# Performance work log

Hardware: AMD Instinct MI355X
Metric: run time of the kernel (lower is better)

The kernel has to match this reference:

```python
import jax, jax.numpy as jnp
import numpy as np

N = 50000      # nodes
E = 600000     # edges
D = 128        # embedding_dim
H = 256        # GENConv MLP hidden = 2*D (expansion=2, num_layers=2)
L = 2          # n_layers
EPS_MSG = 1e-7
EPS_NORM = 1e-5


def setup_inputs() -> dict:
    key = jax.random.key(0)
    ks = jax.random.split(key, 16)
    s = 0.05
    inp = {}
    inp["x"] = jax.random.normal(ks[0], (N, 1), jnp.float32)
    inp["edge_index"] = jax.random.randint(ks[1], (2, E), 0, N)
    inp["edge_attr"] = jax.random.normal(ks[2], (E, 1), jnp.float32)
    # encoders
    inp["Wn"] = jax.random.normal(ks[3], (1, D), jnp.float32) * s
    inp["bn_b"] = jnp.zeros((D,), jnp.float32)
    inp["We"] = jax.random.normal(ks[4], (1, D), jnp.float32) * s
    inp["be"] = jnp.zeros((D,), jnp.float32)
    # per-layer BatchNorm affine
    inp["bn_gamma"] = jnp.ones((L, D), jnp.float32)
    inp["bn_beta"] = jnp.zeros((L, D), jnp.float32)
    # per-layer GENConv params: learnable temperature t, MLP [D->H->D] with LayerNorm
    inp["t"] = jnp.ones((L,), jnp.float32)
    inp["W1"] = jax.random.normal(ks[5], (L, D, H), jnp.float32) * s
    inp["b1"] = jnp.zeros((L, H), jnp.float32)
    inp["ln_g"] = jnp.ones((L, H), jnp.float32)
    inp["ln_b"] = jnp.zeros((L, H), jnp.float32)
    inp["W2"] = jax.random.normal(ks[6], (L, H, D), jnp.float32) * s
    inp["b2"] = jnp.zeros((L, D), jnp.float32)
    return inp


def _segment_softmax(logits, seg, num):
    # per-channel softmax over edges grouped by destination node
    m = jax.ops.segment_max(logits, seg, num_segments=num)
    m = jnp.where(jnp.isfinite(m), m, 0.0)  # empty segments
    ex = jnp.exp(logits - m[seg])
    den = jax.ops.segment_sum(ex, seg, num_segments=num)
    return ex / (den[seg] + 1e-16)


def reference(x, edge_index, edge_attr, Wn, bn_b, We, be,
              bn_gamma, bn_beta, t, W1, b1, ln_g, ln_b, W2, b2):
    src, dst = edge_index[0], edge_index[1]
    h = x @ Wn + bn_b                 # [N, D] node encoder
    e = edge_attr @ We + be           # [E, D] edge encoder
    for l in range(L):
        # DeepGCNLayer 'res+': h_in -> BN -> ReLU -> conv -> + h_in
        mu = h.mean(axis=0)
        var = h.var(axis=0)
        hn = (h - mu) / jnp.sqrt(var + EPS_NORM) * bn_gamma[l] + bn_beta[l]
        hn = jax.nn.relu(hn)
        # GENConv: msg = relu(x_j + e) + eps; softmax-aggr with temperature t
        msg = jax.nn.relu(hn[src] + e) + EPS_MSG          # [E, D]
        alpha = _segment_softmax(msg * t[l], dst, N)      # [E, D]
        agg = jax.ops.segment_sum(msg * alpha, dst, num_segments=N)  # [N, D]
        out = agg + hn                                    # add root
        # GENConv MLP: Linear -> LayerNorm -> ReLU -> Linear
        z = out @ W1[l] + b1[l]
        zm = z.mean(axis=-1, keepdims=True)
        zv = z.var(axis=-1, keepdims=True)
        z = (z - zm) / jnp.sqrt(zv + EPS_NORM) * ln_g[l] + ln_b[l]
        z = jax.nn.relu(z)
        z = z @ W2[l] + b2[l]
        h = h + z                                         # res+ residual
    # DotProductPredictor over the same edge list
    return (h[src] * h[dst]).sum(axis=-1)                 # [E]
```

## Files before the change

### kernel.cpp

```cpp
#include <hip/hip_runtime.h>
#include <hip/hip_bf16.h>
#include <math.h>

#define NN 50000
#define NE 600000
#define MPAD 50048
#define NHS (MPAD / 16)
#define DIM 128
#define HID 256
#define NB 49
#define HIST_BLOCKS ((NE + 255) / 256)
#define CAST_BLOCKS ((4 * DIM * HID) / 256)
#define EPS_MSG 1e-7f
#define EPS_NORM 1e-5f
#define MLPW_WAVES 3
#define MLPW_THREADS (MLPW_WAVES * 64)

typedef __attribute__((ext_vector_type(8))) short short8v;
typedef __attribute__((ext_vector_type(8))) unsigned short ushort8v;
typedef __attribute__((ext_vector_type(4))) float f32x4;

__device__ inline ushort f2bf(float f) {
    union { float f; unsigned u; } v; v.f = f;
    unsigned r = v.u + 0x7FFF + ((v.u >> 16) & 1);
    return (ushort)(r >> 16);
}
__device__ inline float bf2f(ushort u) {
    union { unsigned u; float f; } v; v.u = (unsigned)u << 16; return v.f;
}

__global__ __launch_bounds__(256) void k_setup(const float* __restrict__ x,
                                               const int* __restrict__ dst,
                                               const float* __restrict__ W1,
                                               const float* __restrict__ W2,
                                               float* __restrict__ xs,
                                               int* __restrict__ deg,
                                               ushort* __restrict__ W1t,
                                               ushort* __restrict__ W2t) {
    int b = blockIdx.x;
    if (b < 64) {
        int lane = threadIdx.x & 63;
        float s = 0.f, q = 0.f;
        for (int i = b * 256 + threadIdx.x; i < NN; i += 64 * 256) {
            float v = x[i];
            s += v; q += v * v;
        }
        #pragma unroll
        for (int off = 32; off >= 1; off >>= 1) {
            s += __shfl_xor(s, off, 64);
            q += __shfl_xor(q, off, 64);
        }
        if (lane == 0) { atomicAdd(&xs[0], s); atomicAdd(&xs[1], q); }
    } else if (b < 64 + HIST_BLOCKS) {
        int i = (b - 64) * 256 + threadIdx.x;
        if (i < NE) atomicAdd(&deg[dst[i]], 1);
    } else {
        const int chunk = DIM * HID;
        int i = (b - 64 - HIST_BLOCKS) * 256 + threadIdx.x;
        int w = i / chunk;
        int j = i - w * chunk;
        if (w < 2) {
            int r = j / HID, c = j - r * HID;
            W1t[(size_t)w * chunk + (size_t)c * DIM + r] = f2bf(W1[(size_t)w * chunk + j]);
        } else {
            int l = w - 2;
            int r = j / DIM, c = j - r * DIM;
            W2t[(size_t)l * chunk + (size_t)c * HID + r] = f2bf(W2[(size_t)l * chunk + j]);
        }
    }
}

__global__ void k_hn0(const float* __restrict__ x, const float* __restrict__ xs,
                      const float* __restrict__ Wn, const float* __restrict__ bnb,
                      const float* __restrict__ gamma, const float* __restrict__ beta,
                      ushort* __restrict__ hn, int total4) {
    int i = blockIdx.x * blockDim.x + threadIdx.x;
    if (i >= total4) return;
    int d4 = (i & 31) * 4;
    int n = i >> 5;
    float mx = xs[0] * (1.f / NN);
    float vx = xs[1] * (1.f / NN) - mx * mx;
    float xv = x[n];
    float4 w = *(const float4*)(Wn + d4);
    float4 b = *(const float4*)(bnb + d4);
    float4 g = *(const float4*)(gamma + d4);
    float4 bt = *(const float4*)(beta + d4);
    ushort4 o;
    {
        float mu = fmaf(mx, w.x, b.x), sc = rsqrtf(vx * w.x * w.x + EPS_NORM) * g.x;
        o.x = f2bf(fmaxf(fmaf(fmaf(xv, w.x, b.x) - mu, sc, bt.x), 0.f));
    }
    {
        float mu = fmaf(mx, w.y, b.y), sc = rsqrtf(vx * w.y * w.y + EPS_NORM) * g.y;
        o.y = f2bf(fmaxf(fmaf(fmaf(xv, w.y, b.y) - mu, sc, bt.y), 0.f));
    }
    {
        float mu = fmaf(mx, w.z, b.z), sc = rsqrtf(vx * w.z * w.z + EPS_NORM) * g.z;
        o.z = f2bf(fmaxf(fmaf(fmaf(xv, w.z, b.z) - mu, sc, bt.z), 0.f));
    }
    {
        float mu = fmaf(mx, w.w, b.w), sc = rsqrtf(vx * w.w * w.w + EPS_NORM) * g.w;
        o.w = f2bf(fmaxf(fmaf(fmaf(xv, w.w, b.w) - mu, sc, bt.w), 0.f));
    }
    *(ushort4*)(hn + (size_t)n * DIM + d4) = o;
}

__global__ __launch_bounds__(256) void k_scanA(const int* __restrict__ deg,
                                               int* __restrict__ partials, int n) {
    __shared__ int ws[4];
    int b = blockIdx.x;
    int t = threadIdx.x;
    int s = 0;
    #pragma unroll
    for (int i = 0; i < 4; ++i) {
        int idx = b * 1024 + t + i * 256;
        s += (idx < n) ? deg[idx] : 0;
    }
    #pragma unroll
    for (int off = 32; off >= 1; off >>= 1) s += __shfl_xor(s, off, 64);
    if ((t & 63) == 0) ws[t >> 6] = s;
    __syncthreads();
    if (t == 0) partials[b] = ws[0] + ws[1] + ws[2] + ws[3];
}

__global__ __launch_bounds__(64) void k_scanB(const int* __restrict__ partials,
                                              int* __restrict__ base,
                                              int* __restrict__ row_off) {
    int t = threadIdx.x;
    int v = (t < NB) ? partials[t] : 0;
    int x = v;
    #pragma unroll
    for (int off = 1; off < 64; off <<= 1) {
        int y = __shfl_up(x, off, 64);
        if (t >= off) x += y;
    }
    if (t < NB) base[t] = x - v;
    if (t == 0) row_off[NN] = NE;
}

__global__ __launch_bounds__(1024) void k_scanC(const int* __restrict__ deg,
                                                const int* __restrict__ base,
                                                int* __restrict__ row_off,
                                                int* __restrict__ cursor, int n) {
    __shared__ int wsum[16];
    int i = blockIdx.x * 1024 + threadIdx.x;
    int lane = threadIdx.x & 63;
    int wid = threadIdx.x >> 6;
    int v = (i < n) ? deg[i] : 0;
    int x = v;
    #pragma unroll
    for (int off = 1; off < 64; off <<= 1) {
        int y = __shfl_up(x, off, 64);
        if (lane >= off) x += y;
    }
    if (lane == 63) wsum[wid] = x;
    __syncthreads();
    if (wid == 0 && lane < 16) {
        int w = wsum[lane];
        #pragma unroll
        for (int off = 1; off < 16; off <<= 1) {
            int y = __shfl_up(w, off, 64);
            if (lane >= off) w += y;
        }
        wsum[lane] = w;
    }
    __syncthreads();
    int prev = (wid == 0) ? 0 : wsum[wid - 1];
    int excl = base[blockIdx.x] + prev + (x - v);
    if (i < n) { row_off[i] = excl; cursor[i] = excl; }
}

__global__ void k_scatter(const int* __restrict__ src, const int* __restrict__ dst,
                          const float* __restrict__ eattr, int* __restrict__ cursor,
                          unsigned long long* __restrict__ erec, int E) {
    int i = blockIdx.x * blockDim.x + threadIdx.x;
    if (i >= E) return;
    int d = dst[i];
    int pos = atomicAdd(&cursor[d], 1);
    unsigned long long r = (unsigned long long)(unsigned)src[i]
                         | ((unsigned long long)(unsigned)i << 16)
                         | ((unsigned long long)f2bf(eattr[i]) << 36);
    erec[pos] = r;
}

__global__ void k_bn_relu(const ushort* __restrict__ hb, const float* __restrict__ stats,
                          const float* __restrict__ gamma, const float* __restrict__ beta,
                          ushort* __restrict__ hn, int total4) {
    int i = blockIdx.x * blockDim.x + threadIdx.x;
    if (i >= total4) return;
    int d4 = (i & 31) * 4;
    int n = i >> 5;
    ushort4 hv = *(const ushort4*)(hb + (size_t)n * DIM + d4);
    float4 s = *(const float4*)(stats + d4);
    float4 q = *(const float4*)(stats + DIM + d4);
    float4 g = *(const float4*)(gamma + d4);
    float4 bt = *(const float4*)(beta + d4);
    ushort4 o;
    {
        float mu = s.x * (1.f / NN), var = q.x * (1.f / NN) - mu * mu;
        float sc = rsqrtf(var + EPS_NORM) * g.x;
        o.x = f2bf(fmaxf(fmaf(bf2f(hv.x) - mu, sc, bt.x), 0.f));
    }
    {
        float mu = s.y * (1.f / NN), var = q.y * (1.f / NN) - mu * mu;
        float sc = rsqrtf(var + EPS_NORM) * g.y;
        o.y = f2bf(fmaxf(fmaf(bf2f(hv.y) - mu, sc, bt.y), 0.f));
    }
    {
        float mu = s.z * (1.f / NN), var = q.z * (1.f / NN) - mu * mu;
        float sc = rsqrtf(var + EPS_NORM) * g.z;
        o.z = f2bf(fmaxf(fmaf(bf2f(hv.z) - mu, sc, bt.z), 0.f));
    }
    {
        float mu = s.w * (1.f / NN), var = q.w * (1.f / NN) - mu * mu;
        float sc = rsqrtf(var + EPS_NORM) * g.w;
        o.w = f2bf(fmaxf(fmaf(bf2f(hv.w) - mu, sc, bt.w), 0.f));
    }
    *(ushort4*)(hn + (size_t)n * DIM + d4) = o;
}

__global__ __launch_bounds__(256) void k_agg(const ushort* __restrict__ hn,
                                             const unsigned long long* __restrict__ erec,
                                             const int* __restrict__ row_off,
                                             const float* __restrict__ We,
                                             const float* __restrict__ be,
                                             const float* __restrict__ t_all, int l,
                                             ushort* __restrict__ ob, int N) {
    int n = blockIdx.x * 4 + (threadIdx.x >> 6);
    if (n >= N) return;
    int lane = threadIdx.x & 63;
    int d0 = lane * 2;
    float2 we = *(const float2*)(We + d0);
    float2 bd = *(const float2*)(be + d0);
    float t = t_all[l];
    int p0 = row_off[n], p1 = row_off[n + 1];
    int deg = p1 - p0;

    int mp = p0 + lane;
    unsigned long long r_l = (mp < p1) ? erec[mp] : 0ull;

    float den0 = 0.f, num0 = 0.f, den1 = 0.f, num1 = 0.f;
    int kmax = deg < 64 ? deg : 64;
    int k = 0;
    for (; k + 8 <= kmax; k += 8) {
        int ss[8]; float ee[8]; uint hv[8];
        #pragma unroll
        for (int u = 0; u < 8; ++u) {
            unsigned long long r = __shfl(r_l, k + u, 64);
            ss[u] = (int)(r & 0xFFFF);
            ee[u] = bf2f((ushort)(r >> 36));
        }
        #pragma unroll
        for (int u = 0; u < 8; ++u)
            hv[u] = *(const uint*)(hn + (size_t)ss[u] * DIM + d0);
        #pragma unroll
        for (int u = 0; u < 8; ++u) {
            float m0 = fmaxf(bf2f((ushort)hv[u]) + fmaf(ee[u], we.x, bd.x), 0.f) + EPS_MSG;
            float m1 = fmaxf(bf2f((ushort)(hv[u] >> 16)) + fmaf(ee[u], we.y, bd.y), 0.f) + EPS_MSG;
            float x0 = __expf(m0 * t), x1 = __expf(m1 * t);
            den0 += x0; num0 += m0 * x0; den1 += x1; num1 += m1 * x1;
        }
    }
    for (; k < kmax; ++k) {
        unsigned long long r = __shfl(r_l, k, 64);
        int s = (int)(r & 0xFFFF);
        float ea = bf2f((ushort)(r >> 36));
        uint hv = *(const uint*)(hn + (size_t)s * DIM + d0);
        float m0 = fmaxf(bf2f((ushort)hv) + fmaf(ea, we.x, bd.x), 0.f) + EPS_MSG;
        float m1 = fmaxf(bf2f((ushort)(hv >> 16)) + fmaf(ea, we.y, bd.y), 0.f) + EPS_MSG;
        float x0 = __expf(m0 * t), x1 = __expf(m1 * t);
        den0 += x0; num0 += m0 * x0; den1 += x1; num1 += m1 * x1;
    }
    for (int p = p0 + 64; p < p1; ++p) {
        unsigned long long r = erec[p];
        int s = (int)(r & 0xFFFF);
        float ea = bf2f((ushort)(r >> 36));
        uint hv = *(const uint*)(hn + (size_t)s * DIM + d0);
        float m0 = fmaxf(bf2f((ushort)hv) + fmaf(ea, we.x, bd.x), 0.f) + EPS_MSG;
        float m1 = fmaxf(bf2f((ushort)(hv >> 16)) + fmaf(ea, we.y, bd.y), 0.f) + EPS_MSG;
        float x0 = __expf(m0 * t), x1 = __expf(m1 * t);
        den0 += x0; num0 += m0 * x0; den1 += x1; num1 += m1 * x1;
    }
    uint hr = *(const uint*)(hn + (size_t)n * DIM + d0);
    float a0 = (deg > 0) ? num0 / (den0 + 1e-16f) : 0.f;
    float a1 = (deg > 0) ? num1 / (den1 + 1e-16f) : 0.f;
    uint o = (uint)f2bf(a0 + bf2f((ushort)hr)) |
             ((uint)f2bf(a1 + bf2f((ushort)(hr >> 16))) << 16);
    *(uint*)(ob + (size_t)n * DIM + d0) = o;
}

template <int FIRST>
__global__ __launch_bounds__(MLPW_THREADS, 1) void k_mlpw(const ushort* __restrict__ A,
                                                          const ushort* __restrict__ B1t,
                                                          const float* __restrict__ b1,
                                                          const float* __restrict__ g,
                                                          const float* __restrict__ bv,
                                                          const ushort* __restrict__ B2t,
                                                          const float* __restrict__ b2,
                                                          const float* __restrict__ x,
                                                          const float* __restrict__ Wn,
                                                          const float* __restrict__ bnb,
                                                          const ushort* hbin,
                                                          ushort* hbout,
                                                          float* __restrict__ stats) {
    __shared__ ushort W1s[256 * 128];
    __shared__ ushort W2s[128 * 256];
    __shared__ ushort Zs[MLPW_WAVES][16 * 256];
    const int tid = threadIdx.x;
    const int lane = tid & 63;
    const int wid = tid >> 6;
    const int l15 = lane & 15;
    const int lq = lane >> 4;
    char* const w1b = (char*)W1s;
    char* const w2b = (char*)W2s;
    char* const zb = (char*)Zs[wid];

    for (int c = tid; c < 4096; c += MLPW_THREADS) {
        int r = c >> 4;
        int cb = (c & 15) * 16;
        *(short8v*)(w1b + r * 256 + (cb ^ ((r & 15) << 4))) =
            *(const short8v*)(B1t + r * 128 + cb / 2);
    }
    for (int c = tid; c < 4096; c += MLPW_THREADS) {
        int r = c >> 5;
        int cb = (c & 31) * 16;
        *(short8v*)(w2b + r * 512 + (cb ^ ((r & 15) << 4))) =
            *(const short8v*)(B2t + r * 256 + cb / 2);
    }
    float bb[16], gg[16], lb[16];
    #pragma unroll
    for (int nf = 0; nf < 16; ++nf) {
        int col = nf * 16 + l15;
        bb[nf] = b1[col]; gg[nf] = g[col]; lb[nf] = bv[col];
    }
    float b2v[8], wnc[8], bnc[8];
    #pragma unroll
    for (int nf = 0; nf < 8; ++nf) {
        int col = nf * 16 + l15;
        b2v[nf] = b2[col];
        wnc[nf] = FIRST ? Wn[col] : 0.f;
        bnc[nf] = FIRST ? bnb[col] : 0.f;
    }
    float ss[8] = {}, sqv[8] = {};
    __syncthreads();

    for (int hs = blockIdx.x * MLPW_WAVES + wid; hs < NHS; hs += 256 * MLPW_WAVES) {
        const int row0 = hs * 16;
        short8v afr[4];
        #pragma unroll
        for (int ks = 0; ks < 4; ++ks)
            afr[ks] = *(const short8v*)(A + (size_t)(row0 + l15) * DIM + ks * 32 + lq * 8);
        f32x4 acc[16] = {};
        #pragma unroll
        for (int ks = 0; ks < 4; ++ks) {
            int cb = (ks * 64 + lq * 16) ^ (l15 << 4);
            #pragma unroll
            for (int nf = 0; nf < 16; ++nf) {
                short8v bfr = *(const short8v*)(w1b + (nf * 16 + l15) * 256 + cb);
                acc[nf] = __builtin_amdgcn_mfma_f32_16x16x32_bf16(afr[ks], bfr, acc[nf],
                                                                  0, 0, 0);
            }
        }
        #pragma unroll
        for (int j = 0; j < 4; ++j) {
            float sum = 0.f, sq = 0.f;
            #pragma unroll
            for (int nf = 0; nf < 16; ++nf) {
                float v = acc[nf][j] + bb[nf];
                acc[nf][j] = v;
                sum += v; sq += v * v;
            }
            #pragma unroll
            for (int off = 1; off <= 8; off <<= 1) {
                sum += __shfl_xor(sum, off, 64);
                sq += __shfl_xor(sq, off, 64);
            }
            float mu = sum * (1.f / HID);
            float var = sq * (1.f / HID) - mu * mu;
            float rs = rsqrtf(var + EPS_NORM);
            int row = lq * 4 + j;
            #pragma unroll
            for (int nf = 0; nf < 16; ++nf) {
                float v = fmaxf(fmaf((acc[nf][j] - mu) * rs, gg[nf], lb[nf]), 0.f);
                int cbz = ((nf * 16 + l15) * 2) ^ ((row & 15) << 4);
                *(ushort*)(zb + row * 512 + cbz) = f2bf(v);
            }
        }
        short8v az[8];
        #pragma unroll
        for (int ks = 0; ks < 8; ++ks)
            az[ks] = *(const short8v*)(zb + l15 * 512 + ((ks * 64 + lq * 16) ^ (l15 << 4)));
        f32x4 acc2[8] = {};
        #pragma unroll
        for (int ks = 0; ks < 8; ++ks) {
            int cb = (ks * 64 + lq * 16) ^ (l15 << 4);
            #pragma unroll
            for (int nf = 0; nf < 8; ++nf) {
                short8v bfr = *(const short8v*)(w2b + (nf * 16 + l15) * 512 + cb);
                acc2[nf] = __builtin_amdgcn_mfma_f32_16x16x32_bf16(az[ks], bfr, acc2[nf],
                                                                   0, 0, 0);
            }
        }
        #pragma unroll
        for (int j = 0; j < 4; ++j) {
            int gr = row0 + lq * 4 + j;
            float xb = 0.f;
            if (FIRST) xb = (gr < NN) ? x[gr] : 0.f;
            size_t rbase = (size_t)gr * DIM;
            bool ok = gr < NN;
            #pragma unroll
            for (int nf = 0; nf < 8; ++nf) {
                int col = nf * 16 + l15;
                float base = FIRST ? fmaf(xb, wnc[nf], bnc[nf]) : bf2f(hbin[rbase + col]);
                float v = acc2[nf][j] + b2v[nf] + base;
                hbout[rbase + col] = f2bf(v);
                if (FIRST) {
                    ss[nf] += ok ? v : 0.f;
                    sqv[nf] += ok ? v * v : 0.f;
                }
            }
        }
    }
    if (FIRST) {
        #pragma unroll
        for (int nf = 0; nf < 8; ++nf) {
            float s = ss[nf], q = sqv[nf];
            s += __shfl_xor(s, 16, 64); s += __shfl_xor(s, 32, 64);
            q += __shfl_xor(q, 16, 64); q += __shfl_xor(q, 32, 64);
            if (lq == 0) {
                int col = nf * 16 + l15;
                atomicAdd(&stats[col], s);
                atomicAdd(&stats[DIM + col], q);
            }
        }
    }
}

__global__ __launch_bounds__(256) void k_dot(const ushort* __restrict__ hb,
                                             const unsigned long long* __restrict__ erec,
                                             const int* __restrict__ row_off,
                                             float* __restrict__ out, int N) {
    int n = blockIdx.x * 4 + (threadIdx.x >> 6);
    if (n >= N) return;
    int lane = threadIdx.x & 63;
    int sub = lane >> 4;
    int l16 = lane & 15;
    float hd[8];
    {
        ushort8v hv = *(const ushort8v*)(hb + (size_t)n * DIM + l16 * 8);
        #pragma unroll
        for (int j = 0; j < 8; ++j) hd[j] = bf2f(hv[j]);
    }
    int p0 = row_off[n], p1 = row_off[n + 1];
    int deg = p1 - p0;
    int mp = p0 + lane;
    unsigned long long r_l = (mp < p1) ? erec[mp] : 0ull;
    int kmax = deg < 64 ? deg : 64;
    for (int k = 0; k < kmax; k += 4) {
        int idx = k + sub;
        bool ok = idx < kmax;
        unsigned long long r = __shfl(r_l, idx, 64);
        int s = (int)(r & 0xFFFF);
        int e = (int)((r >> 16) & 0xFFFFF);
        ushort8v av = *(const ushort8v*)(hb + (size_t)(ok ? s : n) * DIM + l16 * 8);
        float p = 0.f;
        #pragma unroll
        for (int j = 0; j < 8; ++j) p = fmaf(bf2f(av[j]), hd[j], p);
        p += __shfl_xor(p, 1, 16);
        p += __shfl_xor(p, 2, 16);
        p += __shfl_xor(p, 4, 16);
        p += __shfl_xor(p, 8, 16);
        if (ok && l16 == 0) out[e] = p;
    }
    for (int pb = p0 + 64; pb < p1; pb += 4) {
        int pe = pb + sub;
        bool ok = pe < p1;
        int s = n, e = 0;
        if (ok) {
            unsigned long long r = erec[pe];
            s = (int)(r & 0xFFFF);
            e = (int)((r >> 16) & 0xFFFFF);
        }
        ushort8v av = *(const ushort8v*)(hb + (size_t)s * DIM + l16 * 8);
        float p = 0.f;
        #pragma unroll
        for (int j = 0; j < 8; ++j) p = fmaf(bf2f(av[j]), hd[j], p);
        p += __shfl_xor(p, 1, 16);
        p += __shfl_xor(p, 2, 16);
        p += __shfl_xor(p, 4, 16);
        p += __shfl_xor(p, 8, 16);
        if (ok && l16 == 0) out[e] = p;
    }
}

extern "C" void kernel_launch(void* const* d_in, const int* in_sizes, int n_in,
                              void* d_out, int out_size, void* d_ws, size_t ws_size,
                              hipStream_t stream) {
    const float* x        = (const float*)d_in[0];
    const int*   ei       = (const int*)d_in[1];
    const float* eattr    = (const float*)d_in[2];
    const float* Wn       = (const float*)d_in[3];
    const float* bnb      = (const float*)d_in[4];
    const float* We       = (const float*)d_in[5];
    const float* be       = (const float*)d_in[6];
    const float* bn_gamma = (const float*)d_in[7];
    const float* bn_beta  = (const float*)d_in[8];
    const float* t_all    = (const float*)d_in[9];
    const float* W1       = (const float*)d_in[10];
    const float* b1       = (const float*)d_in[11];
    const float* ln_g     = (const float*)d_in[12];
    const float* ln_b     = (const float*)d_in[13];
    const float* W2       = (const float*)d_in[14];
    const float* b2       = (const float*)d_in[15];
    float* out = (float*)d_out;

    const int N = NN, E = NE, D = DIM, H = HID;
    const int* src = ei;
    const int* dst = ei + E;

    char* ws = (char*)d_ws;
    auto alloc = [&](size_t bytes) {
        char* p = ws;
        ws += (bytes + 255) & ~(size_t)255;
        return p;
    };
    ushort* ob      = (ushort*)alloc((size_t)MPAD * D * 2);
    ushort* hn      = (ushort*)alloc((size_t)MPAD * D * 2);
    ushort* hb      = (ushort*)alloc((size_t)MPAD * D * 2);
    ushort* W1t     = (ushort*)alloc((size_t)2 * D * H * 2);
    ushort* W2t     = (ushort*)alloc((size_t)2 * D * H * 2);
    unsigned long long* erec = (unsigned long long*)alloc((size_t)E * 8);
    int*    row_off = (int*)alloc((size_t)(N + 1) * 4);
    int*    cursor  = (int*)alloc((size_t)N * 4);
    int*    deg     = (int*)alloc((size_t)N * 4);
    int*    partials= (int*)alloc((size_t)64 * 4);
    int*    pbase   = (int*)alloc((size_t)64 * 4);
    float*  stats   = (float*)alloc((size_t)2 * D * 4);
    float*  xs      = (float*)alloc((size_t)2 * 4);

    hipMemsetAsync(deg, 0, (size_t)N * 4, stream);
    hipMemsetAsync(stats, 0, 1024 + 8, stream);

    k_setup<<<64 + HIST_BLOCKS + CAST_BLOCKS, 256, 0, stream>>>(x, dst, W1, W2,
                                                                xs, deg, W1t, W2t);
    k_scanA<<<NB, 256, 0, stream>>>(deg, partials, N);
    k_scanB<<<1, 64, 0, stream>>>(partials, pbase, row_off);
    k_scanC<<<NB, 1024, 0, stream>>>(deg, pbase, row_off, cursor, N);
    k_scatter<<<(E + 255) / 256, 256, 0, stream>>>(src, dst, eattr, cursor, erec, E);
    k_hn0<<<(N * 32 + 255) / 256, 256, 0, stream>>>(x, xs, Wn, bnb, bn_gamma, bn_beta,
                                                    hn, N * 32);

    k_agg<<<(N + 3) / 4, 256, 0, stream>>>(hn, erec, row_off, We, be, t_all, 0, ob, N);
    k_mlpw<1><<<256, MLPW_THREADS, 0, stream>>>(ob, W1t, b1, ln_g, ln_b, W2t, b2,
                                                x, Wn, bnb, hb, hb, stats);
    k_bn_relu<<<(N * 32 + 255) / 256, 256, 0, stream>>>(hb, stats, bn_gamma + D,
                                                        bn_beta + D, hn, N * 32);

    k_agg<<<(N + 3) / 4, 256, 0, stream>>>(hn, erec, row_off, We, be, t_all, 1, ob, N);
    k_mlpw<0><<<256, MLPW_THREADS, 0, stream>>>(ob, W1t + (size_t)D * H, b1 + H,
                                                ln_g + H, ln_b + H, W2t + (size_t)D * H,
                                                b2 + D, x, Wn, bnb, hb, hb, stats);

    k_dot<<<(N + 3) / 4, 256, 0, stream>>>(hb, erec, row_off, out, N);
}
```

Baseline: 431.4 us.

## Split fused MLP kernel into two GEMM kernels with global intermediate

```diff
diff --git a/kernel.cpp b/kernel.cpp
--- a/kernel.cpp
+++ b/kernel.cpp
@@ -13,8 +13,6 @@
 #define CAST_BLOCKS ((4 * DIM * HID) / 256)
 #define EPS_MSG 1e-7f
 #define EPS_NORM 1e-5f
-#define MLPW_WAVES 3
-#define MLPW_THREADS (MLPW_WAVES * 64)
 
 typedef __attribute__((ext_vector_type(8))) short short8v;
 typedef __attribute__((ext_vector_type(8))) unsigned short ushort8v;
@@ -289,147 +287,169 @@
     *(uint*)(ob + (size_t)n * DIM + d0) = o;
 }
 
-template <int FIRST>
-__global__ __launch_bounds__(MLPW_THREADS, 1) void k_mlpw(const ushort* __restrict__ A,
-                                                          const ushort* __restrict__ B1t,
-                                                          const float* __restrict__ b1,
-                                                          const float* __restrict__ g,
-                                                          const float* __restrict__ bv,
-                                                          const ushort* __restrict__ B2t,
-                                                          const float* __restrict__ b2,
-                                                          const float* __restrict__ x,
-                                                          const float* __restrict__ Wn,
-                                                          const float* __restrict__ bnb,
-                                                          const ushort* hbin,
-                                                          ushort* hbout,
-                                                          float* __restrict__ stats) {
+__global__ __launch_bounds__(512, 4) void k_z1(const ushort* __restrict__ A,
+                                               const ushort* __restrict__ B1t,
+                                               const float* __restrict__ b1,
+                                               ushort* __restrict__ z,
+                                               float2* __restrict__ murs) {
     __shared__ ushort W1s[256 * 128];
-    __shared__ ushort W2s[128 * 256];
-    __shared__ ushort Zs[MLPW_WAVES][16 * 256];
     const int tid = threadIdx.x;
     const int lane = tid & 63;
     const int wid = tid >> 6;
     const int l15 = lane & 15;
     const int lq = lane >> 4;
     char* const w1b = (char*)W1s;
-    char* const w2b = (char*)W2s;
-    char* const zb = (char*)Zs[wid];
-
-    for (int c = tid; c < 4096; c += MLPW_THREADS) {
+
+    for (int c = tid; c < 4096; c += 512) {
         int r = c >> 4;
         int cb = (c & 15) * 16;
         *(short8v*)(w1b + r * 256 + (cb ^ ((r & 15) << 4))) =
             *(const short8v*)(B1t + r * 128 + cb / 2);
     }
-    for (int c = tid; c < 4096; c += MLPW_THREADS) {
+    __syncthreads();
+
+    int s = blockIdx.x * 8 + wid;
+    if (s >= NHS) return;
+    const int row0 = s * 16;
+
+    short8v afr[4];
+    #pragma unroll
+    for (int ks = 0; ks < 4; ++ks)
+        afr[ks] = *(const short8v*)(A + (size_t)(row0 + l15) * DIM + ks * 32 + lq * 8);
+
+    float rsum[4] = {}, rsq[4] = {};
+    ushort* zrow = z + (size_t)(row0 + lq * 4) * HID + l15;
+    #pragma unroll
+    for (int ct = 0; ct < 16; ++ct) {
+        f32x4 acc = {};
+        int cb = 0 ^ (l15 << 4);
+        #pragma unroll
+        for (int ks = 0; ks < 4; ++ks) {
+            short8v bfr = *(const short8v*)(w1b + (ct * 16 + l15) * 256 +
+                                            ((ks * 64 + lq * 16) ^ (l15 << 4)));
+            acc = __builtin_amdgcn_mfma_f32_16x16x32_bf16(afr[ks], bfr, acc, 0, 0, 0);
+        }
+        (void)cb;
+        float bbv = b1[ct * 16 + l15];
+        #pragma unroll
+        for (int j = 0; j < 4; ++j) {
+            float zv = acc[j] + bbv;
+            rsum[j] += zv; rsq[j] += zv * zv;
+            zrow[(size_t)j * HID + ct * 16] = f2bf(zv);
+        }
+    }
+    #pragma unroll
+    for (int j = 0; j < 4; ++j) {
+        float sm = rsum[j], q = rsq[j];
+        sm += __shfl_xor(sm, 1, 16); q += __shfl_xor(q, 1, 16);
+        sm += __shfl_xor(sm, 2, 16); q += __shfl_xor(q, 2, 16);
+        sm += __shfl_xor(sm, 4, 16); q += __shfl_xor(q, 4, 16);
+        sm += __shfl_xor(sm, 8, 16); q += __shfl_xor(q, 8, 16);
+        if (l15 == 0) {
+            float mu = sm * (1.f / HID);
+            float var = q * (1.f / HID) - mu * mu;
+            murs[row0 + lq * 4 + j] = make_float2(mu, rsqrtf(var + EPS_NORM));
+        }
+    }
+}
+
+template <int FIRST>
+__global__ __launch_bounds__(512, 4) void k_z2(const ushort* __restrict__ z,
+                                               const float2* __restrict__ murs,
+                                               const float* __restrict__ g,
+                                               const float* __restrict__ lb,
+                                               const ushort* __restrict__ B2t,
+                                               const float* __restrict__ b2,
+                                               const float* __restrict__ x,
+                                               const float* __restrict__ Wn,
+                                               const float* __restrict__ bnb,
+                                               const ushort* hbin,
+                                               ushort* hbout,
+                                               float* __restrict__ stats) {
+    __shared__ ushort W2s[128 * 256];
+    const int tid = threadIdx.x;
+    const int lane = tid & 63;
+    const int wid = tid >> 6;
+    const int l15 = lane & 15;
+    const int lq = lane >> 4;
+    char* const w2b = (char*)W2s;
+
+    for (int c = tid; c < 4096; c += 512) {
         int r = c >> 5;
         int cb = (c & 31) * 16;
         *(short8v*)(w2b + r * 512 + (cb ^ ((r & 15) << 4))) =
             *(const short8v*)(B2t + r * 256 + cb / 2);
     }
-    float bb[16], gg[16], lb[16];
-    #pragma unroll
-    for (int nf = 0; nf < 16; ++nf) {
-        int col = nf * 16 + l15;
-        bb[nf] = b1[col]; gg[nf] = g[col]; lb[nf] = bv[col];
-    }
-    float b2v[8], wnc[8], bnc[8];
-    #pragma unroll
-    for (int nf = 0; nf < 8; ++nf) {
-        int col = nf * 16 + l15;
-        b2v[nf] = b2[col];
-        wnc[nf] = FIRST ? Wn[col] : 0.f;
-        bnc[nf] = FIRST ? bnb[col] : 0.f;
-    }
+    __syncthreads();
+
+    int s = blockIdx.x * 8 + wid;
+    if (s >= NHS) return;
+    const int row0 = s * 16;
+
+    float2 mr = murs[row0 + l15];
+    short8v af2[8];
+    #pragma unroll
+    for (int ks = 0; ks < 8; ++ks) {
+        ushort8v zr = *(const ushort8v*)(z + (size_t)(row0 + l15) * HID + ks * 32 + lq * 8);
+        float4 g0 = *(const float4*)(g + ks * 32 + lq * 8);
+        float4 g1 = *(const float4*)(g + ks * 32 + lq * 8 + 4);
+        float4 l0 = *(const float4*)(lb + ks * 32 + lq * 8);
+        float4 l1 = *(const float4*)(lb + ks * 32 + lq * 8 + 4);
+        ushort8v o;
+        o[0] = f2bf(fmaxf(fmaf((bf2f(zr[0]) - mr.x) * mr.y, g0.x, l0.x), 0.f));
+        o[1] = f2bf(fmaxf(fmaf((bf2f(zr[1]) - mr.x) * mr.y, g0.y, l0.y), 0.f));
+        o[2] = f2bf(fmaxf(fmaf((bf2f(zr[2]) - mr.x) * mr.y, g0.z, l0.z), 0.f));
+        o[3] = f2bf(fmaxf(fmaf((bf2f(zr[3]) - mr.x) * mr.y, g0.w, l0.w), 0.f));
+        o[4] = f2bf(fmaxf(fmaf((bf2f(zr[4]) - mr.x) * mr.y, g1.x, l1.x), 0.f));
+        o[5] = f2bf(fmaxf(fmaf((bf2f(zr[5]) - mr.x) * mr.y, g1.y, l1.y), 0.f));
+        o[6] = f2bf(fmaxf(fmaf((bf2f(zr[6]) - mr.x) * mr.y, g1.z, l1.z), 0.f));
+        o[7] = f2bf(fmaxf(fmaf((bf2f(zr[7]) - mr.x) * mr.y, g1.w, l1.w), 0.f));
+        af2[ks] = (short8v)o;
+    }
+
     float ss[8] = {}, sqv[8] = {};
-    __syncthreads();
-
-    for (int hs = blockIdx.x * MLPW_WAVES + wid; hs < NHS; hs += 256 * MLPW_WAVES) {
-        const int row0 = hs * 16;
-        short8v afr[4];
-        #pragma unroll
-        for (int ks = 0; ks < 4; ++ks)
-            afr[ks] = *(const short8v*)(A + (size_t)(row0 + l15) * DIM + ks * 32 + lq * 8);
-        f32x4 acc[16] = {};
-        #pragma unroll
-        for (int ks = 0; ks < 4; ++ks) {
-            int cb = (ks * 64 + lq * 16) ^ (l15 << 4);
-            #pragma unroll
-            for (int nf = 0; nf < 16; ++nf) {
-                short8v bfr = *(const short8v*)(w1b + (nf * 16 + l15) * 256 + cb);
-                acc[nf] = __builtin_amdgcn_mfma_f32_16x16x32_bf16(afr[ks], bfr, acc[nf],
-                                                                  0, 0, 0);
-            }
-        }
-        #pragma unroll
-        for (int j = 0; j < 4; ++j) {
-            float sum = 0.f, sq = 0.f;
-            #pragma unroll
-            for (int nf = 0; nf < 16; ++nf) {
-                float v = acc[nf][j] + bb[nf];
-                acc[nf][j] = v;
-                sum += v; sq += v * v;
-            }
-            #pragma unroll
-            for (int off = 1; off <= 8; off <<= 1) {
-                sum += __shfl_xor(sum, off, 64);
-                sq += __shfl_xor(sq, off, 64);
-            }
-            float mu = sum * (1.f / HID);
-            float var = sq * (1.f / HID) - mu * mu;
-            float rs = rsqrtf(var + EPS_NORM);
-            int row = lq * 4 + j;
-            #pragma unroll
-            for (int nf = 0; nf < 16; ++nf) {
-                float v = fmaxf(fmaf((acc[nf][j] - mu) * rs, gg[nf], lb[nf]), 0.f);
-                int cbz = ((nf * 16 + l15) * 2) ^ ((row & 15) << 4);
-                *(ushort*)(zb + row * 512 + cbz) = f2bf(v);
-            }
-        }
-        short8v az[8];
-        #pragma unroll
-        for (int ks = 0; ks < 8; ++ks)
-            az[ks] = *(const short8v*)(zb + l15 * 512 + ((ks * 64 + lq * 16) ^ (l15 << 4)));
-        f32x4 acc2[8] = {};
+    #pragma unroll
+    for (int ct = 0; ct < 8; ++ct) {
+        f32x4 acc = {};
         #pragma unroll
         for (int ks = 0; ks < 8; ++ks) {
-            int cb = (ks * 64 + lq * 16) ^ (l15 << 4);
-            #pragma unroll
-            for (int nf = 0; nf < 8; ++nf) {
-                short8v bfr = *(const short8v*)(w2b + (nf * 16 + l15) * 512 + cb);
-                acc2[nf] = __builtin_amdgcn_mfma_f32_16x16x32_bf16(az[ks], bfr, acc2[nf],
-                                                                   0, 0, 0);
-            }
-        }
+            short8v bfr = *(const short8v*)(w2b + (ct * 16 + l15) * 512 +
+                                            ((ks * 64 + lq * 16) ^ (l15 << 4)));
+            acc = __builtin_amdgcn_mfma_f32_16x16x32_bf16(af2[ks], bfr, acc, 0, 0, 0);
+        }
+        int col = ct * 16 + l15;
+        float bvv = b2[col];
+        float wnc = FIRST ? Wn[col] : 0.f;
+        float bnc = FIRST ? bnb[col] : 0.f;
         #pragma unroll
         for (int j = 0; j < 4; ++j) {
             int gr = row0 + lq * 4 + j;
-            float xb = 0.f;
-            if (FIRST) xb = (gr < NN) ? x[gr] : 0.f;
-            size_t rbase = (size_t)gr * DIM;
-            bool ok = gr < NN;
-            #pragma unroll
-            for (int nf = 0; nf < 8; ++nf) {
-                int col = nf * 16 + l15;
-                float base = FIRST ? fmaf(xb, wnc[nf], bnc[nf]) : bf2f(hbin[rbase + col]);
-                float v = acc2[nf][j] + b2v[nf] + base;
-                hbout[rbase + col] = f2bf(v);
-                if (FIRST) {
-                    ss[nf] += ok ? v : 0.f;
-                    sqv[nf] += ok ? v * v : 0.f;
-                }
+            size_t idx = (size_t)gr * DIM + col;
+            float base;
+            if (FIRST) {
+                float xv = (gr < NN) ? x[gr] : 0.f;
+                base = fmaf(xv, wnc, bnc);
+            } else {
+                base = bf2f(hbin[idx]);
             }
+            float v = acc[j] + bvv + base;
+            hbout[idx] = f2bf(v);
+            if (FIRST) {
+                bool ok = gr < NN;
+                ss[ct] += ok ? v : 0.f;
+                sqv[ct] += ok ? v * v : 0.f;
+            }
         }
     }
     if (FIRST) {
         #pragma unroll
-        for (int nf = 0; nf < 8; ++nf) {
-            float s = ss[nf], q = sqv[nf];
-            s += __shfl_xor(s, 16, 64); s += __shfl_xor(s, 32, 64);
+        for (int ct = 0; ct < 8; ++ct) {
+            float sm = ss[ct], q = sqv[ct];
+            sm += __shfl_xor(sm, 16, 64); sm += __shfl_xor(sm, 32, 64);
             q += __shfl_xor(q, 16, 64); q += __shfl_xor(q, 32, 64);
             if (lq == 0) {
-                int col = nf * 16 + l15;
-                atomicAdd(&stats[col], s);
+                int col = ct * 16 + l15;
+                atomicAdd(&stats[col], sm);
                 atomicAdd(&stats[DIM + col], q);
             }
         }
@@ -527,6 +547,8 @@
     ushort* ob      = (ushort*)alloc((size_t)MPAD * D * 2);
     ushort* hn      = (ushort*)alloc((size_t)MPAD * D * 2);
     ushort* hb      = (ushort*)alloc((size_t)MPAD * D * 2);
+    ushort* z       = (ushort*)alloc((size_t)MPAD * H * 2);
+    float2* murs    = (float2*)alloc((size_t)MPAD * 8);
     ushort* W1t     = (ushort*)alloc((size_t)2 * D * H * 2);
     ushort* W2t     = (ushort*)alloc((size_t)2 * D * H * 2);
     unsigned long long* erec = (unsigned long long*)alloc((size_t)E * 8);
@@ -551,15 +573,17 @@
                                                     hn, N * 32);
 
     k_agg<<<(N + 3) / 4, 256, 0, stream>>>(hn, erec, row_off, We, be, t_all, 0, ob, N);
-    k_mlpw<1><<<256, MLPW_THREADS, 0, stream>>>(ob, W1t, b1, ln_g, ln_b, W2t, b2,
-                                                x, Wn, bnb, hb, hb, stats);
+    k_z1<<<NHS / 8, 512, 0, stream>>>(ob, W1t, b1, z, murs);
+    k_z2<1><<<NHS / 8, 512, 0, stream>>>(z, murs, ln_g, ln_b, W2t, b2,
+                                         x, Wn, bnb, hb, hb, stats);
     k_bn_relu<<<(N * 32 + 255) / 256, 256, 0, stream>>>(hb, stats, bn_gamma + D,
                                                         bn_beta + D, hn, N * 32);
 
     k_agg<<<(N + 3) / 4, 256, 0, stream>>>(hn, erec, row_off, We, be, t_all, 1, ob, N);
-    k_mlpw<0><<<256, MLPW_THREADS, 0, stream>>>(ob, W1t + (size_t)D * H, b1 + H,
-                                                ln_g + H, ln_b + H, W2t + (size_t)D * H,
-                                                b2 + D, x, Wn, bnb, hb, hb, stats);
+    k_z1<<<NHS / 8, 512, 0, stream>>>(ob, W1t + (size_t)D * H, b1 + H, z, murs);
+    k_z2<0><<<NHS / 8, 512, 0, stream>>>(z, murs, ln_g + H, ln_b + H,
+                                         W2t + (size_t)D * H, b2 + D,
+                                         x, Wn, bnb, hb, hb, stats);
 
     k_dot<<<(N + 3) / 4, 256, 0, stream>>>(hb, erec, row_off, out, N);
 }
```

After: 417.6 us. -3.2%, faster.
